# Kernel tuning notes

Measured on AMD Instinct MI355X. Metric: run time of the kernel, lower is better.

Reference implementation:

```python
import jax, jax.numpy as jnp
import numpy as np

B, N, Q, C, R, D, E = 16, 500, 25, 80, 3, 512, 3072
HOPS = 5


def setup_inputs() -> dict:
    key = jax.random.key(0)
    ks = jax.random.split(key, 16)
    s = 0.02
    return {
        'nodes_elmo': jax.random.normal(ks[0], (B, N, 3, 1024), jnp.float32),
        'query_elmo': jax.random.normal(ks[1], (B, Q, 3, 1024), jnp.float32),
        'adj': (jax.random.uniform(ks[2], (B, R, N, N)) < 0.05).astype(jnp.float32),
        'mask': jax.random.randint(ks[3], (B, C, N), 0, 2).astype(jnp.int32),
        'nodes_length': jax.random.randint(ks[4], (B,), 1, N + 1).astype(jnp.int32),
        'query_length': jax.random.randint(ks[5], (B,), 1, Q + 1).astype(jnp.int32),
        'Wq': jax.random.normal(ks[6], (E, D)) * s, 'bq': jnp.zeros((D,)),
        'Wn': jax.random.normal(ks[7], (E, D)) * s, 'bn': jnp.zeros((D,)),
        'Wh': jax.random.normal(ks[8], (D, D)) * s, 'bh': jnp.zeros((D,)),
        'Wc': jax.random.normal(ks[9], (2 * D, D)) * s, 'bc': jnp.zeros((D,)),
        'Wa': jax.random.normal(ks[10], (3 * D,)) * s,
        'Wo1': jax.random.normal(ks[11], (4 * D, 128)) * s, 'bo1': jnp.zeros((128,)),
        'Wo2': jax.random.normal(ks[12], (128, 1)) * s, 'bo2': jnp.zeros((1,)),
    }


def _forward(nodes_elmo, query_elmo, adj, mask_f, nodes_length,
             Wq, bq, Wn, bn, Wh, bh, Wc, bc, Wa, Wo1, bo1, Wo2, bo2):
    # feature layer (linear query encoding; dropout is eval/no-op)
    query = query_elmo.reshape(B, Q, E) @ Wq + bq            # [B,Q,D]
    nodes_compress = jnp.tanh(nodes_elmo.reshape(B, N, E) @ Wn + bn)  # [B,N,D]
    nmask = (jnp.arange(N)[None, :] < nodes_length[:, None]).astype(jnp.float32)[..., None]  # [B,N,1]
    nodes = nodes_compress * nmask

    # relational GCN: hidden_linears = [same Linear]*4 -> one shared (Wh,bh)
    last = nodes
    for _ in range(HOPS):
        h = (last @ Wh + bh) * nmask                          # [B,N,D] (shared across rels + self)
        # sum_r adj[:,r] @ h  (all per-relation hidden tensors are identical) + self term
        update = jnp.einsum('brnm,bmd->bnd', adj, h) + h
        att = jax.nn.sigmoid(jnp.concatenate([update, last], -1) @ Wc + bc) * nmask
        last = att * jnp.tanh(update) + (1.0 - att) * last

    # bi-attention: linear over concat([nodes,query,nodes*query]) decomposed into 3 dot products
    wn_, wq_, ws_ = Wa[:D], Wa[D:2 * D], Wa[2 * D:]
    sim = (last @ wn_)[:, :, None] + (query @ wq_)[:, None, :] \
        + jnp.einsum('bnd,bqd->bnq', last * ws_, query)       # [B,N,Q]
    n2q = jax.nn.softmax(sim, -1) @ query                     # [B,N,D]
    b_att = jax.nn.softmax(sim.max(-1), -1)                   # [B,N]
    q2n = jnp.einsum('bn,bnd->bd', b_att, nodes_compress)[:, None, :]  # [B,1,D]
    g = jnp.concatenate([nodes_compress, n2q, nodes_compress * n2q,
                         nodes_compress * q2n], -1)           # [B,N,4D]

    # output layer
    raw = (jnp.tanh(g @ Wo1 + bo1) @ Wo2 + bo2)[..., 0]       # [B,N]
    p2 = mask_f * raw[:, None, :]                             # [B,C,N]
    p2 = jnp.where(p2 == 0, -jnp.inf, p2)
    return p2.max(-1)                                         # [B,C]


def reference(nodes_elmo, query_elmo, adj, mask, nodes_length, query_length,
              Wq, bq, Wn, bn, Wh, bh, Wc, bc, Wa, Wo1, bo1, Wo2, bo2):
    return _forward(nodes_elmo, query_elmo, adj, mask.astype(jnp.float32), nodes_length,
                    Wq, bq, Wn, bn, Wh, bh, Wc, bc, Wa, Wo1, bo1, Wo2, bo2)
```

## Files before the change

kernel.cpp:

```cpp
#include <hip/hip_runtime.h>
#include <hip/hip_bf16.h>
#include <math.h>

#define BB 16
#define NN 500
#define QQ 25
#define CC 80
#define RR 3
#define DD 512
#define EE 3072
#define HOPS 5
#define MROWS (BB*NN)

typedef float f32x4  __attribute__((ext_vector_type(4)));
typedef short s16x8  __attribute__((ext_vector_type(8)));
typedef short s16x4  __attribute__((ext_vector_type(4)));

static __device__ __forceinline__ short f2bf(float x) {
    __hip_bfloat16 h = __float2bfloat16(x);
    return __builtin_bit_cast(short, h);
}
static __device__ __forceinline__ float bf2f(short s) {
    __hip_bfloat16 h = __builtin_bit_cast(__hip_bfloat16, s);
    return __bfloat162float(h);
}

template<int MODE, int KT, int BM>
__global__ __launch_bounds__(256)
void gemm_mfma(const float* __restrict__ Af,
               const short* __restrict__ Ab, const short* __restrict__ Ab2,
               const short* __restrict__ Bt, const float* __restrict__ bias,
               float* __restrict__ Cf, short* __restrict__ Cb,
               short* __restrict__ Cb2, const float* __restrict__ lastf,
               const short* __restrict__ n2qb, const short* __restrict__ q2nb,
               const float* __restrict__ Wo2, const float* __restrict__ bo2,
               float* __restrict__ rawout,
               const int* __restrict__ nlen,
               int mclamp)
{
    constexpr int MI  = BM / 32;
    constexpr int ACH = BM / 32;
    constexpr int NKT = KT / 64;

    __shared__ short Als[2 * BM * 64];
    __shared__ short Bls[2 * 128 * 64];
    __shared__ float rawp[BM][2];

    const int t    = threadIdx.x;
    const int lane = t & 63;
    const int w    = t >> 6;
    const int wm   = w >> 1;
    const int wn   = w & 1;
    const int n0   = blockIdx.x * 128;
    const int m0   = blockIdx.y * BM;
    const int z    = blockIdx.z;
    const size_t za = (MODE == 3) ? (size_t)z * (512 * 512) : 0;

    int arow[ACH], aslot[ACH], arg_[ACH];
    #pragma unroll
    for (int c = 0; c < ACH; ++c) {
        int f = c * 256 + t;
        arow[c] = f >> 3;  aslot[c] = f & 7;
        int rg = m0 + arow[c]; if (rg > mclamp) rg = mclamp;
        arg_[c] = rg;
    }
    int brow[4], bslot[4];
    #pragma unroll
    for (int c = 0; c < 4; ++c) {
        int f = c * 256 + t;
        brow[c] = f >> 3;  bslot[c] = f & 7;
    }

    f32x4 paf[ACH][2];
    s16x8 pa[ACH], pao[ACH], pb[4];

    auto stage_regs = [&](int kt) {
        #pragma unroll
        for (int c = 0; c < ACH; ++c) {
            int k = kt * 64 + aslot[c] * 8;
            if constexpr (MODE <= 1) {
                const float* s = Af + (size_t)arg_[c] * KT + k;
                paf[c][0] = *(const f32x4*)s;
                paf[c][1] = *(const f32x4*)(s + 4);
            } else if constexpr (MODE == 2) {
                pa[c] = *(const s16x8*)(Ab + (size_t)arg_[c] * 512 + k);
            } else if constexpr (MODE == 3) {
                pa[c] = *(const s16x8*)(Ab + za + (size_t)arg_[c] * 512 + k);
            } else if constexpr (MODE == 4) {
                pa[c] = (k < 512)
                    ? *(const s16x8*)(Ab  + (size_t)arg_[c] * 512 + k)
                    : *(const s16x8*)(Ab2 + (size_t)arg_[c] * 512 + (k - 512));
            } else {
                int seg = k >> 9, off = k & 511;
                const short* p1 = (seg == 1) ? n2qb : Ab;
                pa[c] = *(const s16x8*)(p1 + (size_t)arg_[c] * 512 + off);
                if (seg >= 2) {
                    const short* p2 = (seg == 2)
                        ? n2qb + (size_t)arg_[c] * 512 + off
                        : q2nb + (size_t)(arg_[c] / NN) * 512 + off;
                    pao[c] = *(const s16x8*)p2;
                }
            }
        }
        #pragma unroll
        for (int c = 0; c < 4; ++c) {
            int k = kt * 64 + bslot[c] * 8;
            pb[c] = *(const s16x8*)(Bt + za + (size_t)(n0 + brow[c]) * KT + k);
        }
    };

    auto write_lds = [&](int bsel, int kt) {
        const int offA = bsel * BM * 64, offB = bsel * 128 * 64;
        #pragma unroll
        for (int c = 0; c < ACH; ++c) {
            s16x8 v;
            if constexpr (MODE <= 1) {
                #pragma unroll
                for (int j = 0; j < 4; ++j) {
                    v[j]     = f2bf(paf[c][0][j]);
                    v[4 + j] = f2bf(paf[c][1][j]);
                }
            } else if constexpr (MODE == 5) {
                int k = kt * 64 + aslot[c] * 8;
                int seg = k >> 9;
                v = pa[c];
                if (seg >= 2) {
                    #pragma unroll
                    for (int j = 0; j < 8; ++j)
                        v[j] = f2bf(bf2f(pa[c][j]) * bf2f(pao[c][j]));
                }
            } else {
                v = pa[c];
            }
            *(s16x8*)&Als[offA + arow[c] * 64 + ((aslot[c] ^ (arow[c] & 7)) << 3)] = v;
        }
        #pragma unroll
        for (int c = 0; c < 4; ++c)
            *(s16x8*)&Bls[offB + brow[c] * 64 + ((bslot[c] ^ (brow[c] & 7)) << 3)] = pb[c];
    };

    f32x4 acc[MI][4];
    #pragma unroll
    for (int i = 0; i < MI; ++i)
        #pragma unroll
        for (int j = 0; j < 4; ++j)
            acc[i][j] = (f32x4){0.f, 0.f, 0.f, 0.f};

    auto mfma_step = [&](int bsel) {
        const int offA = bsel * BM * 64, offB = bsel * 128 * 64;
        #pragma unroll
        for (int ks = 0; ks < 2; ++ks) {
            s16x8 af[MI], bfr[4];
            int s = ks * 4 + (lane >> 4);
            #pragma unroll
            for (int i = 0; i < MI; ++i) {
                int ar = wm * (MI * 16) + i * 16 + (lane & 15);
                af[i] = *(const s16x8*)&Als[offA + ar * 64 + ((s ^ (ar & 7)) << 3)];
            }
            #pragma unroll
            for (int j = 0; j < 4; ++j) {
                int br = wn * 64 + j * 16 + (lane & 15);
                bfr[j] = *(const s16x8*)&Bls[offB + br * 64 + ((s ^ (br & 7)) << 3)];
            }
            #pragma unroll
            for (int i = 0; i < MI; ++i)
                #pragma unroll
                for (int j = 0; j < 4; ++j)
                    acc[i][j] = __builtin_amdgcn_mfma_f32_16x16x32_bf16(
                        af[i], bfr[j], acc[i][j], 0, 0, 0);
        }
    };

    stage_regs(0);
    write_lds(0, 0);
    __syncthreads();
    for (int kt = 0; kt < NKT - 1; ++kt) {
        stage_regs(kt + 1);
        mfma_step(kt & 1);
        write_lds((kt + 1) & 1, kt + 1);
        __syncthreads();
    }
    mfma_step((NKT - 1) & 1);

    if constexpr (MODE == 5) {
        #pragma unroll
        for (int mi = 0; mi < MI; ++mi) {
            #pragma unroll
            for (int r = 0; r < 4; ++r) {
                float s = 0.f;
                #pragma unroll
                for (int ni = 0; ni < 4; ++ni) {
                    int col = wn * 64 + ni * 16 + (lane & 15);
                    float hv = tanhf(acc[mi][ni][r] + bias[col]);
                    s += hv * Wo2[col];
                }
                #pragma unroll
                for (int o = 1; o <= 8; o <<= 1) s += __shfl_xor(s, o, 64);
                if ((lane & 15) == 0)
                    rawp[wm * (MI * 16) + mi * 16 + ((lane >> 4) << 2) + r][wn] = s;
            }
        }
        __syncthreads();
        if (t < BM) {
            int m = m0 + t;
            if (m < MROWS) rawout[m] = rawp[t][0] + rawp[t][1] + bo2[0];
        }
        return;
    }

    #pragma unroll
    for (int mi = 0; mi < MI; ++mi) {
        #pragma unroll
        for (int ni = 0; ni < 4; ++ni) {
            f32x4 v = acc[mi][ni];
            int col   = n0 + wn * 64 + ni * 16 + (lane & 15);
            int rbase = m0 + wm * (MI * 16) + mi * 16 + ((lane >> 4) << 2);
            if constexpr (MODE == 2) {
                if (rbase < MROWS) {
                    int b0 = rbase / NN, nr = rbase - b0 * NN;
                    if (nr + 3 < NN && rbase + 3 < MROWS) {
                        int len = nlen[b0];
                        s16x4 pk;
                        #pragma unroll
                        for (int r = 0; r < 4; ++r) {
                            float nm = (nr + r < len) ? 1.f : 0.f;
                            pk[r] = f2bf((v[r] + bias[col]) * nm);
                        }
                        *(s16x4*)&Cb[((size_t)(b0 * 512 + col)) * 512 + nr] = pk;
                    } else {
                        #pragma unroll
                        for (int r = 0; r < 4; ++r) {
                            int row = rbase + r;
                            if (row < MROWS) {
                                int b = row / NN, n = row - b * NN;
                                float nm = (n < nlen[b]) ? 1.f : 0.f;
                                Cb[((size_t)(b * 512 + col)) * 512 + n] =
                                    f2bf((v[r] + bias[col]) * nm);
                            }
                        }
                    }
                }
            } else {
                #pragma unroll
                for (int r = 0; r < 4; ++r) {
                    int row = rbase + r;
                    float x = v[r];
                    if constexpr (MODE == 0) {
                        if (row < 400) Cb[(size_t)row * 512 + col] = f2bf(x + bias[col]);
                    } else if constexpr (MODE == 1) {
                        if (row < MROWS) {
                            int b = row / NN, n = row - b * NN;
                            float nm = (n < nlen[b]) ? 1.f : 0.f;
                            float tv = tanhf(x + bias[col]);
                            size_t idx = (size_t)row * 512 + col;
                            Cb[idx] = f2bf(tv);
                            float lm = tv * nm;
                            Cf[idx] = lm;  Cb2[idx] = f2bf(lm);
                        }
                    } else if constexpr (MODE == 3) {
                        if (row < NN)
                            Cb[((size_t)z * NN + row) * 512 + col] = f2bf(x);
                    } else if constexpr (MODE == 4) {
                        if (row < MROWS) {
                            int b = row / NN, n = row - b * NN;
                            float nm = (n < nlen[b]) ? 1.f : 0.f;
                            size_t idx = (size_t)row * 512 + col;
                            float att = nm / (1.f + expf(-(x + bias[col])));
                            float u = bf2f(Ab[idx]);
                            float l = lastf[idx];
                            float o = att * tanhf(u) + (1.f - att) * l;
                            Cf[idx] = o;  Cb[idx] = f2bf(o);
                        }
                    }
                }
            }
        }
    }
}

__global__ __launch_bounds__(256)
void wtrans_all(const float* __restrict__ W0, const float* __restrict__ W1,
                const float* __restrict__ W2, const float* __restrict__ W3,
                const float* __restrict__ W4,
                short* __restrict__ O0, short* __restrict__ O1,
                short* __restrict__ O2, short* __restrict__ O3,
                short* __restrict__ O4)
{
    const int z = blockIdx.z;
    int K, N; const float* W; short* O;
    if      (z == 0) { K = 3072; N = 512; W = W0; O = O0; }
    else if (z == 1) { K = 3072; N = 512; W = W1; O = O1; }
    else if (z == 2) { K = 512;  N = 512; W = W2; O = O2; }
    else if (z == 3) { K = 1024; N = 512; W = W3; O = O3; }
    else             { K = 2048; N = 128; W = W4; O = O4; }
    int n0 = blockIdx.x * 32, k0 = blockIdx.y * 32;
    if (n0 >= N || k0 >= K) return;
    __shared__ float tile[32][33];
    int tx = threadIdx.x, ty = threadIdx.y;
    for (int i = ty; i < 32; i += 8)
        tile[i][tx] = W[(size_t)(k0 + i) * N + n0 + tx];
    __syncthreads();
    for (int i = ty; i < 32; i += 8)
        O[(size_t)(n0 + i) * K + k0 + tx] = f2bf(tile[tx][i]);
}

__global__ __launch_bounds__(256)
void adjsum_conv(const float* __restrict__ adj, short* __restrict__ out)
{
    int i = blockIdx.x * 256 + threadIdx.x;
    int b = i >> 18;
    int rem = i & (512 * 512 - 1);
    int n = rem >> 9, m = rem & 511;
    float v = 0.f;
    if (n < NN && m < NN) {
        const float* base = adj + (((size_t)b * RR) * NN + n) * NN + m;
        v = base[0] + base[(size_t)NN * NN] + base[2 * (size_t)NN * NN];
        if (n == m) v += 1.f;
    }
    out[i] = f2bf(v);
}

__global__ __launch_bounds__(256)
void sim_n2q2(const float* __restrict__ last_f, const short* __restrict__ query_b,
              const float* __restrict__ Wa, short* __restrict__ n2q_b,
              float* __restrict__ simmax)
{
    __shared__ short qL[32 * 520];
    __shared__ short cfL[16 * 520];
    __shared__ float pL[16 * 32];

    const int t = threadIdx.x;
    const int b = blockIdx.y;
    const int nbase = blockIdx.x * 16;
    const int nl = t >> 4, c = t & 15;
    const int n = nbase + nl;
    const bool valid = (n < NN);
    const int rowg = b * NN + (valid ? n : NN - 1);

    for (int i = t; i < 1600; i += 256) {
        int q = i >> 6, dc = i & 63;
        s16x8 v = *(const s16x8*)(query_b + ((size_t)b * QQ + q) * 512 + dc * 8);
        *(s16x8*)&qL[q * 520 + dc * 8] = v;
    }

    float apart = 0.f;
    {
        const float* lr = last_f + (size_t)rowg * 512 + c * 32;
        s16x8 pk[4];
        #pragma unroll
        for (int j = 0; j < 32; ++j) {
            int d = c * 32 + j;
            float lv = lr[j];
            apart += lv * Wa[d];
            pk[j >> 3][j & 7] = f2bf(Wa[512 + d] + lv * Wa[1024 + d]);
        }
        #pragma unroll
        for (int jj = 0; jj < 4; ++jj)
            *(s16x8*)&cfL[nl * 520 + c * 32 + jj * 8] = pk[jj];
        #pragma unroll
        for (int o = 1; o <= 8; o <<= 1) apart += __shfl_xor(apart, o, 64);
    }
    __syncthreads();

    float sum1 = 0.f, sum2 = 0.f;
    const bool q2v = (c < 9);
    #pragma unroll 8
    for (int dc = 0; dc < 64; ++dc) {
        s16x8 cf8 = *(const s16x8*)&cfL[nl * 520 + dc * 8];
        s16x8 qa  = *(const s16x8*)&qL[c * 520 + dc * 8];
        s16x8 qb2 = *(const s16x8*)&qL[(c + 16) * 520 + dc * 8];
        #pragma unroll
        for (int e = 0; e < 8; ++e) {
            float cf = bf2f(cf8[e]);
            sum1 += cf * bf2f(qa[e]);
            sum2 += cf * bf2f(qb2[e]);
        }
    }
    float s1 = apart + sum1;
    float s2 = q2v ? (apart + sum2) : -INFINITY;
    float m = fmaxf(s1, s2);
    #pragma unroll
    for (int o = 1; o <= 8; o <<= 1) m = fmaxf(m, __shfl_xor(m, o, 64));
    float e1 = expf(s1 - m);
    float e2 = q2v ? expf(s2 - m) : 0.f;
    float den = e1 + e2;
    #pragma unroll
    for (int o = 1; o <= 8; o <<= 1) den += __shfl_xor(den, o, 64);
    float inv = 1.f / den;
    pL[nl * 32 + c]      = e1 * inv;
    pL[nl * 32 + c + 16] = e2 * inv;
    if (c == 0 && valid) simmax[b * NN + n] = m;
    __syncthreads();

    float accv[4][8];
    #pragma unroll
    for (int jj = 0; jj < 4; ++jj)
        #pragma unroll
        for (int e = 0; e < 8; ++e) accv[jj][e] = 0.f;
    for (int q = 0; q < QQ; ++q) {
        float p = pL[nl * 32 + q];
        #pragma unroll
        for (int jj = 0; jj < 4; ++jj) {
            s16x8 q8 = *(const s16x8*)&qL[q * 520 + (jj * 16 + c) * 8];
            #pragma unroll
            for (int e = 0; e < 8; ++e) accv[jj][e] += p * bf2f(q8[e]);
        }
    }
    if (valid) {
        #pragma unroll
        for (int jj = 0; jj < 4; ++jj) {
            s16x8 o8;
            #pragma unroll
            for (int e = 0; e < 8; ++e) o8[e] = f2bf(accv[jj][e]);
            *(s16x8*)(n2q_b + ((size_t)b * NN + n) * 512 + jj * 128 + c * 8) = o8;
        }
    }
}

__global__ __launch_bounds__(256)
void batt_q2n2(const float* __restrict__ simmax, const short* __restrict__ nc_b,
               short* __restrict__ q2n_b)
{
    __shared__ float pL[NN];
    __shared__ float red[4];
    __shared__ float part[4][64];
    const int b = blockIdx.y, d0 = blockIdx.x * 64;
    const int t = threadIdx.x, wv = t >> 6, lane = t & 63;
    const float* sm = simmax + (size_t)b * NN;

    float m = -INFINITY;
    for (int n = t; n < NN; n += 256) m = fmaxf(m, sm[n]);
    #pragma unroll
    for (int o = 32; o >= 1; o >>= 1) m = fmaxf(m, __shfl_xor(m, o, 64));
    if (lane == 0) red[wv] = m;
    __syncthreads();
    float M4 = fmaxf(fmaxf(red[0], red[1]), fmaxf(red[2], red[3]));
    __syncthreads();

    float den = 0.f;
    for (int n = t; n < NN; n += 256) { float e = expf(sm[n] - M4); pL[n] = e; den += e; }
    #pragma unroll
    for (int o = 32; o >= 1; o >>= 1) den += __shfl_xor(den, o, 64);
    if (lane == 0) red[wv] = den;
    __syncthreads();
    float invD = 1.f / (red[0] + red[1] + red[2] + red[3]);

    int d = d0 + (t & 63);
    int pi = t >> 6;
    float acc = 0.f;
    for (int n = pi * 125; n < pi * 125 + 125; ++n)
        acc += pL[n] * bf2f(nc_b[((size_t)b * NN + n) * 512 + d]);
    part[pi][t & 63] = acc;
    __syncthreads();
    if (t < 64)
        q2n_b[(size_t)b * 512 + d0 + t] =
            f2bf((part[0][t] + part[1][t] + part[2][t] + part[3][t]) * invD);
}

__global__ __launch_bounds__(64)
void out_kernel(const int* __restrict__ mask, const float* __restrict__ raw,
                float* __restrict__ out)
{
    int bc = blockIdx.x;
    int b  = bc / CC;
    int lane = threadIdx.x;
    const int*   mrow = mask + (size_t)bc * NN;
    const float* rrow = raw  + (size_t)b * NN;
    float mx = -INFINITY;
    for (int n = lane; n < NN; n += 64) {
        float v = (float)mrow[n] * rrow[n];
        v = (v == 0.f) ? -INFINITY : v;
        mx = fmaxf(mx, v);
    }
    #pragma unroll
    for (int o = 32; o >= 1; o >>= 1) mx = fmaxf(mx, __shfl_xor(mx, o, 64));
    if (lane == 0) out[bc] = mx;
}

extern "C" void kernel_launch(void* const* d_in, const int* in_sizes, int n_in,
                              void* d_out, int out_size, void* d_ws, size_t ws_size,
                              hipStream_t stream)
{
    const float* nodes_elmo = (const float*)d_in[0];
    const float* query_elmo = (const float*)d_in[1];
    const float* adj        = (const float*)d_in[2];
    const int*   mask       = (const int*)  d_in[3];
    const int*   nlen       = (const int*)  d_in[4];
    const float* Wq  = (const float*)d_in[6];
    const float* bq  = (const float*)d_in[7];
    const float* Wn  = (const float*)d_in[8];
    const float* bn  = (const float*)d_in[9];
    const float* Wh  = (const float*)d_in[10];
    const float* bh  = (const float*)d_in[11];
    const float* Wc  = (const float*)d_in[12];
    const float* bc  = (const float*)d_in[13];
    const float* Wa  = (const float*)d_in[14];
    const float* Wo1 = (const float*)d_in[15];
    const float* bo1 = (const float*)d_in[16];
    const float* Wo2 = (const float*)d_in[17];
    const float* bo2 = (const float*)d_in[18];
    float* out = (float*)d_out;

    char* p = (char*)d_ws;
    auto carveF = [&](size_t n) { float* r = (float*)p; p += n * 4; return r; };
    auto carveS = [&](size_t n) { short* r = (short*)p; p += n * 2; return r; };

    float* last_f0   = carveF((size_t)MROWS * 512);
    float* last_f1   = carveF((size_t)MROWS * 512);
    float* simmax    = carveF(MROWS);
    float* raw       = carveF(MROWS + 64);
    short* query_b   = carveS((size_t)400 * 512);
    short* nc_b      = carveS((size_t)MROWS * 512);
    short* last_b0   = carveS((size_t)MROWS * 512);
    short* last_b1   = carveS((size_t)MROWS * 512);
    short* hT_b      = carveS((size_t)BB * 512 * 512);
    short* update_b  = carveS((size_t)MROWS * 512);
    short* n2q_b     = carveS((size_t)MROWS * 512);
    short* adjsum_b  = carveS((size_t)BB * 512 * 512);
    short* q2n_b     = carveS((size_t)BB * 512);
    short* WqT       = carveS((size_t)512 * 3072);
    short* WnT       = carveS((size_t)512 * 3072);
    short* WhT       = carveS((size_t)512 * 512);
    short* WcT       = carveS((size_t)512 * 1024);
    short* Wo1T      = carveS((size_t)128 * 2048);

    wtrans_all<<<dim3(16, 96, 5), dim3(32, 8), 0, stream>>>(
        Wq, Wn, Wh, Wc, Wo1, WqT, WnT, WhT, WcT, Wo1T);

    adjsum_conv<<<(BB * 512 * 512) / 256, 256, 0, stream>>>(adj, adjsum_b);

    gemm_mfma<0, 3072, 64><<<dim3(4, 7), 256, 0, stream>>>(
        query_elmo, nullptr, nullptr, WqT, bq, nullptr, query_b, nullptr,
        nullptr, nullptr, nullptr, nullptr, nullptr, nullptr, nullptr, 399);

    gemm_mfma<1, 3072, 128><<<dim3(4, 63), 256, 0, stream>>>(
        nodes_elmo, nullptr, nullptr, WnT, bn, last_f0, nc_b, last_b0,
        nullptr, nullptr, nullptr, nullptr, nullptr, nullptr, nlen, MROWS - 1);

    float* lf_cur = last_f0; float* lf_nxt = last_f1;
    short* lb_cur = last_b0; short* lb_nxt = last_b1;
    for (int hop = 0; hop < HOPS; ++hop) {
        gemm_mfma<2, 512, 64><<<dim3(4, 125), 256, 0, stream>>>(
            nullptr, lb_cur, nullptr, WhT, bh, nullptr, hT_b, nullptr,
            nullptr, nullptr, nullptr, nullptr, nullptr, nullptr, nlen, MROWS - 1);

        gemm_mfma<3, 512, 64><<<dim3(4, 8, 16), 256, 0, stream>>>(
            nullptr, adjsum_b, nullptr, hT_b, nullptr, nullptr, update_b,
            nullptr, nullptr, nullptr, nullptr, nullptr, nullptr, nullptr,
            nullptr, 511);

        gemm_mfma<4, 1024, 64><<<dim3(4, 125), 256, 0, stream>>>(
            nullptr, update_b, lb_cur, WcT, bc, lf_nxt, lb_nxt, nullptr,
            lf_cur, nullptr, nullptr, nullptr, nullptr, nullptr, nlen, MROWS - 1);

        float* tf = lf_cur; lf_cur = lf_nxt; lf_nxt = tf;
        short* ts = lb_cur; lb_cur = lb_nxt; lb_nxt = ts;
    }

    sim_n2q2<<<dim3(32, 16), 256, 0, stream>>>(lf_cur, query_b, Wa, n2q_b, simmax);
    batt_q2n2<<<dim3(8, 16), 256, 0, stream>>>(simmax, nc_b, q2n_b);

    gemm_mfma<5, 2048, 64><<<dim3(1, 125), 256, 0, stream>>>(
        nullptr, nc_b, nullptr, Wo1T, bo1, nullptr, nullptr, nullptr,
        nullptr, n2q_b, q2n_b, Wo2, bo2, raw, nullptr, MROWS - 1);

    out_kernel<<<BB * CC, 64, 0, stream>>>(mask, raw, out);
}
```

Measured before the change: 727.2 us.

## Swizzle GEMM block-to-tile mapping for XCD locality and retile adj and output GEMMs

New measurement: 702.3 us. -3.4%, faster.

```diff
diff --git a/kernel.cpp b/kernel.cpp
--- a/kernel.cpp
+++ b/kernel.cpp
@@ -25,7 +25,7 @@
     return __bfloat162float(h);
 }
 
-template<int MODE, int KT, int BM>
+template<int MODE, int KT, int BM, int SWZ>
 __global__ __launch_bounds__(256)
 void gemm_mfma(const float* __restrict__ Af,
                const short* __restrict__ Ab, const short* __restrict__ Ab2,
@@ -51,9 +51,21 @@
     const int w    = t >> 6;
     const int wm   = w >> 1;
     const int wn   = w & 1;
-    const int n0   = blockIdx.x * 128;
-    const int m0   = blockIdx.y * BM;
-    const int z    = blockIdx.z;
+
+    int m0, n0, z = 0;
+    if constexpr (SWZ == 1) {
+        int id = blockIdx.x, r = id & 7, q = id >> 3;
+        int pan = r + 8 * (q >> 2);
+        n0 = (q & 3) * 128;  m0 = pan * BM;
+        if (m0 > mclamp) return;
+    } else if constexpr (SWZ == 2) {
+        int id = blockIdx.x, r = id & 7, k = id >> 3;
+        z = r + 8 * (k >> 4);
+        int inner = k & 15;
+        m0 = (inner >> 2) * BM;  n0 = (inner & 3) * 128;
+    } else {
+        n0 = blockIdx.x * 128;  m0 = blockIdx.y * BM;  z = blockIdx.z;
+    }
     const size_t za = (MODE == 3) ? (size_t)z * (512 * 512) : 0;
 
     int arow[ACH], aslot[ACH], arg_[ACH];
@@ -529,27 +541,27 @@
 
     adjsum_conv<<<(BB * 512 * 512) / 256, 256, 0, stream>>>(adj, adjsum_b);
 
-    gemm_mfma<0, 3072, 64><<<dim3(4, 7), 256, 0, stream>>>(
+    gemm_mfma<0, 3072, 64, 0><<<dim3(4, 7), 256, 0, stream>>>(
         query_elmo, nullptr, nullptr, WqT, bq, nullptr, query_b, nullptr,
         nullptr, nullptr, nullptr, nullptr, nullptr, nullptr, nullptr, 399);
 
-    gemm_mfma<1, 3072, 128><<<dim3(4, 63), 256, 0, stream>>>(
+    gemm_mfma<1, 3072, 128, 1><<<256, 256, 0, stream>>>(
         nodes_elmo, nullptr, nullptr, WnT, bn, last_f0, nc_b, last_b0,
         nullptr, nullptr, nullptr, nullptr, nullptr, nullptr, nlen, MROWS - 1);
 
     float* lf_cur = last_f0; float* lf_nxt = last_f1;
     short* lb_cur = last_b0; short* lb_nxt = last_b1;
     for (int hop = 0; hop < HOPS; ++hop) {
-        gemm_mfma<2, 512, 64><<<dim3(4, 125), 256, 0, stream>>>(
+        gemm_mfma<2, 512, 64, 1><<<512, 256, 0, stream>>>(
             nullptr, lb_cur, nullptr, WhT, bh, nullptr, hT_b, nullptr,
             nullptr, nullptr, nullptr, nullptr, nullptr, nullptr, nlen, MROWS - 1);
 
-        gemm_mfma<3, 512, 64><<<dim3(4, 8, 16), 256, 0, stream>>>(
+        gemm_mfma<3, 512, 128, 2><<<256, 256, 0, stream>>>(
             nullptr, adjsum_b, nullptr, hT_b, nullptr, nullptr, update_b,
             nullptr, nullptr, nullptr, nullptr, nullptr, nullptr, nullptr,
             nullptr, 511);
 
-        gemm_mfma<4, 1024, 64><<<dim3(4, 125), 256, 0, stream>>>(
+        gemm_mfma<4, 1024, 64, 1><<<512, 256, 0, stream>>>(
             nullptr, update_b, lb_cur, WcT, bc, lf_nxt, lb_nxt, nullptr,
             lf_cur, nullptr, nullptr, nullptr, nullptr, nullptr, nlen, MROWS - 1);
 
@@ -560,7 +572,7 @@
     sim_n2q2<<<dim3(32, 16), 256, 0, stream>>>(lf_cur, query_b, Wa, n2q_b, simmax);
     batt_q2n2<<<dim3(8, 16), 256, 0, stream>>>(simmax, nc_b, q2n_b);
 
-    gemm_mfma<5, 2048, 64><<<dim3(1, 125), 256, 0, stream>>>(
+    gemm_mfma<5, 2048, 32, 0><<<dim3(1, 250), 256, 0, stream>>>(
         nullptr, nc_b, nullptr, Wo1T, bo1, nullptr, nullptr, nullptr,
         nullptr, n2q_b, q2n_b, Wo2, bo2, raw, nullptr, MROWS - 1);
 
```
